# Kernel tuning notes

Hardware: AMD Instinct MI355X
Metric: run time of the kernel (lower is better)

The kernel has to match this reference:

```python
import jax, jax.numpy as jnp
import numpy as np

# Intersection(mode='product'):
#   a_fk = a @ feats.T            # [Na, K]
#   b_fk = b @ feats.T            # [Nb, K]
#   mask = (a_fk[:,None,:] > 0) & (b_fk[None,:,:] > 0)
#   result = sum_k (a_fk[:,None,:] * b_fk[None,:,:]) * mask   # [Na, Nb]
# For the product op, (x*y)*[x>0 & y>0] == relu(x)*relu(y) elementwise
# (any term with a non-positive factor is zeroed either way), so the
# broadcast+mask+reduce collapses exactly into a GEMM over relu'd scores.

def setup_inputs() -> dict:
    key = jax.random.key(0)
    k1, k2, k3 = jax.random.split(key, 3)
    a = jax.random.normal(k1, (1024, 2048), dtype=jnp.float32)
    b = jax.random.normal(k2, (1024, 2048), dtype=jnp.float32)
    feats = jax.random.normal(k3, (128, 2048), dtype=jnp.float32)
    return {"a": a, "b": b, "feats": feats}

def reference(a, b, feats):
    a_fk = a @ feats.T            # [Na, K]
    b_fk = b @ feats.T            # [Nb, K]
    # masked product-intersection reduced over K; identical math to the
    # broadcast (Na, Nb, K) -> sum formulation of the torch module.
    return jnp.einsum('ak,bk->ab', jax.nn.relu(a_fk), jax.nn.relu(b_fk))
```

## Files before the change

### kernel.cpp

```cpp
#include <hip/hip_runtime.h>


typedef __attribute__((ext_vector_type(8))) __bf16 bf16x8;
typedef __attribute__((ext_vector_type(4))) __bf16 bf16x4;
typedef __attribute__((ext_vector_type(4))) float floatx4;

#define KD     2048
#define NF     128
#define NA     1024
#define NPART  16
#define FKN    (2048 * 128)

static __device__ inline bf16x8 cvt8(float4 u, float4 v) {
    bf16x8 s;
    s[0] = (__bf16)u.x; s[1] = (__bf16)u.y; s[2] = (__bf16)u.z; s[3] = (__bf16)u.w;
    s[4] = (__bf16)v.x; s[5] = (__bf16)v.y; s[6] = (__bf16)v.z; s[7] = (__bf16)v.w;
    return s;
}

__global__ __launch_bounds__(256) void gemm1_part(const float* __restrict__ A,
                                                  const float* __restrict__ B,
                                                  const float* __restrict__ F,
                                                  float* __restrict__ part) {
    __shared__ __bf16 Xs[64 * 40];
    __shared__ __bf16 Fs[128 * 40];

    const int t    = threadIdx.x;
    const int m0   = blockIdx.x * 64;
    const int s    = blockIdx.y;
    const int k0   = s * 128;
    const float* src = (m0 < NA) ? (A + (size_t)m0 * KD)
                                 : (B + (size_t)(m0 - NA) * KD);

    const int lane = t & 63;
    const int w    = t >> 6;
    const int ln   = lane & 15;
    const int quad = lane >> 4;
    const int q8   = quad * 8;

    floatx4 acc[4][2];
#pragma unroll
    for (int mt = 0; mt < 4; mt++)
#pragma unroll
        for (int nt = 0; nt < 2; nt++)
            acc[mt][nt] = (floatx4){0.f, 0.f, 0.f, 0.f};

    const int xrow = t >> 2, xcol = (t & 3) * 8;
    const int frow = t >> 1, fcol = (t & 1) * 16;

#pragma unroll
    for (int kk = 0; kk < 128; kk += 32) {
        {
            const float* p = src + (size_t)xrow * KD + (k0 + kk + xcol);
            float4 u = *(const float4*)p;
            float4 v = *(const float4*)(p + 4);
            *(bf16x8*)&Xs[xrow * 40 + xcol] = cvt8(u, v);
        }
        {
            const float* p = F + (size_t)frow * KD + (k0 + kk + fcol);
            float4 u0 = *(const float4*)(p + 0);
            float4 u1 = *(const float4*)(p + 4);
            float4 u2 = *(const float4*)(p + 8);
            float4 u3 = *(const float4*)(p + 12);
            *(bf16x8*)&Fs[frow * 40 + fcol]     = cvt8(u0, u1);
            *(bf16x8*)&Fs[frow * 40 + fcol + 8] = cvt8(u2, u3);
        }
        __syncthreads();

        bf16x8 bfrag[2];
#pragma unroll
        for (int nt = 0; nt < 2; nt++)
            bfrag[nt] = *(const bf16x8*)&Fs[(w * 32 + nt * 16 + ln) * 40 + q8];
#pragma unroll
        for (int mt = 0; mt < 4; mt++) {
            bf16x8 af = *(const bf16x8*)&Xs[(mt * 16 + ln) * 40 + q8];
#pragma unroll
            for (int nt = 0; nt < 2; nt++)
                acc[mt][nt] = __builtin_amdgcn_mfma_f32_16x16x32_bf16(
                    af, bfrag[nt], acc[mt][nt], 0, 0, 0);
        }
        __syncthreads();
    }

    float* pdst = part + (size_t)s * FKN;
#pragma unroll
    for (int mt = 0; mt < 4; mt++)
#pragma unroll
        for (int nt = 0; nt < 2; nt++)
#pragma unroll
            for (int r = 0; r < 4; r++) {
                int row = m0 + mt * 16 + quad * 4 + r;
                int col = w * 32 + nt * 16 + ln;
                pdst[(size_t)row * NF + col] = acc[mt][nt][r];
            }
}

__global__ __launch_bounds__(256) void reduce_relu(const float* __restrict__ part,
                                                   __bf16* __restrict__ fkb) {
    int idx = blockIdx.x * 256 + threadIdx.x;
    size_t base = (size_t)idx * 4;
    float4 sum = make_float4(0.f, 0.f, 0.f, 0.f);
#pragma unroll
    for (int s = 0; s < NPART; s++) {
        float4 u = *(const float4*)(part + (size_t)s * FKN + base);
        sum.x += u.x; sum.y += u.y; sum.z += u.z; sum.w += u.w;
    }
    bf16x4 o;
    o[0] = (__bf16)fmaxf(sum.x, 0.f);
    o[1] = (__bf16)fmaxf(sum.y, 0.f);
    o[2] = (__bf16)fmaxf(sum.z, 0.f);
    o[3] = (__bf16)fmaxf(sum.w, 0.f);
    *(bf16x4*)(fkb + base) = o;
}

__global__ __launch_bounds__(256) void gemm2(const __bf16* __restrict__ fkb,
                                             float* __restrict__ out) {
    __shared__ __bf16 Ps[64 * 136];
    __shared__ __bf16 Qs[64 * 136];

    const int t    = threadIdx.x;
    const int i0   = blockIdx.y * 64;
    const int j0   = blockIdx.x * 64;
    const int lane = t & 63;
    const int w    = t >> 6;
    const int wm   = w & 1;
    const int wn   = w >> 1;
    const int ln   = lane & 15;
    const int quad = lane >> 4;
    const int q8   = quad * 8;

    const int prow = t >> 2, pcol = (t & 3) * 32;
    {
        const __bf16* p = fkb + (size_t)(i0 + prow) * NF + pcol;
        const __bf16* q = fkb + (size_t)(NA + j0 + prow) * NF + pcol;
#pragma unroll
        for (int c = 0; c < 32; c += 8) {
            *(bf16x8*)&Ps[prow * 136 + pcol + c] = *(const bf16x8*)(p + c);
            *(bf16x8*)&Qs[prow * 136 + pcol + c] = *(const bf16x8*)(q + c);
        }
    }
    __syncthreads();

    floatx4 acc[2][2];
#pragma unroll
    for (int mt = 0; mt < 2; mt++)
#pragma unroll
        for (int nt = 0; nt < 2; nt++)
            acc[mt][nt] = (floatx4){0.f, 0.f, 0.f, 0.f};

#pragma unroll
    for (int k0 = 0; k0 < 128; k0 += 32) {
        bf16x8 af[2], bf[2];
#pragma unroll
        for (int mt = 0; mt < 2; mt++)
            af[mt] = *(const bf16x8*)&Ps[(wm * 32 + mt * 16 + ln) * 136 + k0 + q8];
#pragma unroll
        for (int nt = 0; nt < 2; nt++)
            bf[nt] = *(const bf16x8*)&Qs[(wn * 32 + nt * 16 + ln) * 136 + k0 + q8];
#pragma unroll
        for (int mt = 0; mt < 2; mt++)
#pragma unroll
            for (int nt = 0; nt < 2; nt++)
                acc[mt][nt] = __builtin_amdgcn_mfma_f32_16x16x32_bf16(
                    af[mt], bf[nt], acc[mt][nt], 0, 0, 0);
    }

#pragma unroll
    for (int mt = 0; mt < 2; mt++)
#pragma unroll
        for (int nt = 0; nt < 2; nt++)
#pragma unroll
            for (int r = 0; r < 4; r++) {
                int row = i0 + wm * 32 + mt * 16 + quad * 4 + r;
                int col = j0 + wn * 32 + nt * 16 + ln;
                out[(size_t)row * 1024 + col] = acc[mt][nt][r];
            }
}

extern "C" void kernel_launch(void* const* d_in, const int* in_sizes, int n_in,
                              void* d_out, int out_size, void* d_ws, size_t ws_size,
                              hipStream_t stream) {
    const float* a     = (const float*)d_in[0];
    const float* b     = (const float*)d_in[1];
    const float* feats = (const float*)d_in[2];
    float* out = (float*)d_out;

    float*   part = (float*)d_ws;
    __bf16*  fkb  = (__bf16*)((char*)d_ws + (size_t)NPART * FKN * 4);

    gemm1_part<<<dim3(32, NPART), 256, 0, stream>>>(a, b, feats, part);
    reduce_relu<<<256, 256, 0, stream>>>(part, fkb);
    gemm2<<<dim3(16, 16), 256, 0, stream>>>(fkb, out);
}
```

Baseline: 79.36 us.

## Fuse three kernels into one persistent kernel with grid barriers

Merges the split-K projection GEMM, the partial-sum reduction with ReLU, and the output GEMM into a single 256-block, 512-thread kernel. The phases are separated by software grid barriers built on an atomic counter, which is cleared by a memset before launch. The split-K factor drops from 16 to 8, halving the partial-sum traffic. This removes two kernel launches and their gaps, but it relies on all 256 blocks being co-resident and adds spin-wait barrier overhead. It also leaves fewer blocks to parallelise the first GEMM.

New measurement: 121.7 us. +53.4%, slower.

```diff
diff --git a/kernel.cpp b/kernel.cpp
--- a/kernel.cpp
+++ b/kernel.cpp
@@ -3,14 +3,22 @@
 
 typedef __attribute__((ext_vector_type(8))) __bf16 bf16x8;
 typedef __attribute__((ext_vector_type(4))) __bf16 bf16x4;
+typedef __attribute__((ext_vector_type(2))) __bf16 bf16x2;
 typedef __attribute__((ext_vector_type(4))) float floatx4;
 
 #define KD     2048
 #define NF     128
 #define NA     1024
-#define NPART  16
+#define NPART  8
+#define KSPLIT 256
 #define FKN    (2048 * 128)
+#define NBLK   256
 
+static __device__ inline bf16x4 cvt4(float4 u) {
+    bf16x4 s;
+    s[0] = (__bf16)u.x; s[1] = (__bf16)u.y; s[2] = (__bf16)u.z; s[3] = (__bf16)u.w;
+    return s;
+}
 static __device__ inline bf16x8 cvt8(float4 u, float4 v) {
     bf16x8 s;
     s[0] = (__bf16)u.x; s[1] = (__bf16)u.y; s[2] = (__bf16)u.z; s[3] = (__bf16)u.w;
@@ -18,163 +26,143 @@
     return s;
 }
 
-__global__ __launch_bounds__(256) void gemm1_part(const float* __restrict__ A,
-                                                  const float* __restrict__ B,
-                                                  const float* __restrict__ F,
-                                                  float* __restrict__ part) {
-    __shared__ __bf16 Xs[64 * 40];
-    __shared__ __bf16 Fs[128 * 40];
+static __device__ inline void grid_barrier(unsigned* ctr) {
+    __syncthreads();
+    if (threadIdx.x == 0) {
+        __threadfence();
+        atomicAdd(ctr, 1u);
+        while (__hip_atomic_load(ctr, __ATOMIC_RELAXED, __HIP_MEMORY_SCOPE_AGENT) < NBLK)
+            __builtin_amdgcn_s_sleep(2);
+        __threadfence();
+    }
+    __syncthreads();
+}
 
+union SMem {
+    struct { __bf16 Xs[64 * 40];  __bf16 Fs[128 * 40]; } a;
+    struct { __bf16 Ps[64 * 136]; __bf16 Qs[64 * 136]; } c;
+};
+
+__global__ __launch_bounds__(512) void fused(const float* __restrict__ A,
+                                             const float* __restrict__ B,
+                                             const float* __restrict__ F,
+                                             float* __restrict__ part,
+                                             __bf16* __restrict__ fkb,
+                                             float* __restrict__ out,
+                                             unsigned* __restrict__ ctr) {
+    __shared__ SMem sm;
     const int t    = threadIdx.x;
-    const int m0   = blockIdx.x * 64;
-    const int s    = blockIdx.y;
-    const int k0   = s * 128;
-    const float* src = (m0 < NA) ? (A + (size_t)m0 * KD)
-                                 : (B + (size_t)(m0 - NA) * KD);
-
+    const int b    = blockIdx.x;
     const int lane = t & 63;
     const int w    = t >> 6;
     const int ln   = lane & 15;
     const int quad = lane >> 4;
     const int q8   = quad * 8;
 
-    floatx4 acc[4][2];
+    {
+        const int mtile = b & 31;
+        const int split = b >> 5;
+        const int m0    = mtile * 64;
+        const int k0    = split * KSPLIT;
+        const float* src = (m0 < NA) ? (A + (size_t)m0 * KD)
+                                     : (B + (size_t)(m0 - NA) * KD);
+
+        floatx4 acc[4];
 #pragma unroll
-    for (int mt = 0; mt < 4; mt++)
+        for (int mt = 0; mt < 4; mt++) acc[mt] = (floatx4){0.f, 0.f, 0.f, 0.f};
+
+        const int xrow = t >> 3, xcol = (t & 7) * 4;
+        const int frow = t >> 2, fcol = (t & 3) * 8;
+
+        for (int kk = 0; kk < KSPLIT; kk += 32) {
+            {
+                float4 u = *(const float4*)(src + (size_t)xrow * KD + (k0 + kk + xcol));
+                *(bf16x4*)&sm.a.Xs[xrow * 40 + xcol] = cvt4(u);
+            }
+            {
+                const float* p = F + (size_t)frow * KD + (k0 + kk + fcol);
+                float4 u = *(const float4*)p;
+                float4 v = *(const float4*)(p + 4);
+                *(bf16x8*)&sm.a.Fs[frow * 40 + fcol] = cvt8(u, v);
+            }
+            __syncthreads();
+
+            bf16x8 bfrag = *(const bf16x8*)&sm.a.Fs[(w * 16 + ln) * 40 + q8];
 #pragma unroll
-        for (int nt = 0; nt < 2; nt++)
-            acc[mt][nt] = (floatx4){0.f, 0.f, 0.f, 0.f};
+            for (int mt = 0; mt < 4; mt++) {
+                bf16x8 af = *(const bf16x8*)&sm.a.Xs[(mt * 16 + ln) * 40 + q8];
+                acc[mt] = __builtin_amdgcn_mfma_f32_16x16x32_bf16(af, bfrag, acc[mt], 0, 0, 0);
+            }
+            __syncthreads();
+        }
 
-    const int xrow = t >> 2, xcol = (t & 3) * 8;
-    const int frow = t >> 1, fcol = (t & 1) * 16;
+        float* pdst = part + (size_t)split * FKN;
+        const int col = w * 16 + ln;
+#pragma unroll
+        for (int mt = 0; mt < 4; mt++)
+#pragma unroll
+            for (int r = 0; r < 4; r++)
+                pdst[(size_t)(m0 + mt * 16 + quad * 4 + r) * NF + col] = acc[mt][r];
+    }
 
+    grid_barrier(ctr);
+
+    {
+        size_t base = ((size_t)b << 10) + (size_t)t * 2;
+        float sx = 0.f, sy = 0.f;
 #pragma unroll
-    for (int kk = 0; kk < 128; kk += 32) {
+        for (int s = 0; s < NPART; s++) {
+            float2 u = *(const float2*)(part + (size_t)s * FKN + base);
+            sx += u.x; sy += u.y;
+        }
+        bf16x2 o;
+        o[0] = (__bf16)fmaxf(sx, 0.f);
+        o[1] = (__bf16)fmaxf(sy, 0.f);
+        *(bf16x2*)(fkb + base) = o;
+    }
+
+    grid_barrier(ctr + 32);
+
+    {
+        const int i0 = (b >> 4) * 64;
+        const int j0 = (b & 15) * 64;
+        const int wm = w & 1;
+        const int wn = w >> 1;
+
+        const int prow = t >> 3, pcol = (t & 7) * 16;
         {
-            const float* p = src + (size_t)xrow * KD + (k0 + kk + xcol);
-            float4 u = *(const float4*)p;
-            float4 v = *(const float4*)(p + 4);
-            *(bf16x8*)&Xs[xrow * 40 + xcol] = cvt8(u, v);
-        }
-        {
-            const float* p = F + (size_t)frow * KD + (k0 + kk + fcol);
-            float4 u0 = *(const float4*)(p + 0);
-            float4 u1 = *(const float4*)(p + 4);
-            float4 u2 = *(const float4*)(p + 8);
-            float4 u3 = *(const float4*)(p + 12);
-            *(bf16x8*)&Fs[frow * 40 + fcol]     = cvt8(u0, u1);
-            *(bf16x8*)&Fs[frow * 40 + fcol + 8] = cvt8(u2, u3);
+            const __bf16* p = fkb + (size_t)(i0 + prow) * NF + pcol;
+            const __bf16* q = fkb + (size_t)(NA + j0 + prow) * NF + pcol;
+            *(bf16x8*)&sm.c.Ps[prow * 136 + pcol]     = *(const bf16x8*)p;
+            *(bf16x8*)&sm.c.Ps[prow * 136 + pcol + 8] = *(const bf16x8*)(p + 8);
+            *(bf16x8*)&sm.c.Qs[prow * 136 + pcol]     = *(const bf16x8*)q;
+            *(bf16x8*)&sm.c.Qs[prow * 136 + pcol + 8] = *(const bf16x8*)(q + 8);
         }
         __syncthreads();
 
-        bf16x8 bfrag[2];
+        floatx4 acc[2];
 #pragma unroll
-        for (int nt = 0; nt < 2; nt++)
-            bfrag[nt] = *(const bf16x8*)&Fs[(w * 32 + nt * 16 + ln) * 40 + q8];
-#pragma unroll
-        for (int mt = 0; mt < 4; mt++) {
-            bf16x8 af = *(const bf16x8*)&Xs[(mt * 16 + ln) * 40 + q8];
-#pragma unroll
-            for (int nt = 0; nt < 2; nt++)
-                acc[mt][nt] = __builtin_amdgcn_mfma_f32_16x16x32_bf16(
-                    af, bfrag[nt], acc[mt][nt], 0, 0, 0);
-        }
-        __syncthreads();
-    }
-
-    float* pdst = part + (size_t)s * FKN;
-#pragma unroll
-    for (int mt = 0; mt < 4; mt++)
-#pragma unroll
-        for (int nt = 0; nt < 2; nt++)
-#pragma unroll
-            for (int r = 0; r < 4; r++) {
-                int row = m0 + mt * 16 + quad * 4 + r;
-                int col = w * 32 + nt * 16 + ln;
-                pdst[(size_t)row * NF + col] = acc[mt][nt][r];
-            }
-}
-
-__global__ __launch_bounds__(256) void reduce_relu(const float* __restrict__ part,
-                                                   __bf16* __restrict__ fkb) {
-    int idx = blockIdx.x * 256 + threadIdx.x;
-    size_t base = (size_t)idx * 4;
-    float4 sum = make_float4(0.f, 0.f, 0.f, 0.f);
-#pragma unroll
-    for (int s = 0; s < NPART; s++) {
-        float4 u = *(const float4*)(part + (size_t)s * FKN + base);
-        sum.x += u.x; sum.y += u.y; sum.z += u.z; sum.w += u.w;
-    }
-    bf16x4 o;
-    o[0] = (__bf16)fmaxf(sum.x, 0.f);
-    o[1] = (__bf16)fmaxf(sum.y, 0.f);
-    o[2] = (__bf16)fmaxf(sum.z, 0.f);
-    o[3] = (__bf16)fmaxf(sum.w, 0.f);
-    *(bf16x4*)(fkb + base) = o;
-}
-
-__global__ __launch_bounds__(256) void gemm2(const __bf16* __restrict__ fkb,
-                                             float* __restrict__ out) {
-    __shared__ __bf16 Ps[64 * 136];
-    __shared__ __bf16 Qs[64 * 136];
-
-    const int t    = threadIdx.x;
-    const int i0   = blockIdx.y * 64;
-    const int j0   = blockIdx.x * 64;
-    const int lane = t & 63;
-    const int w    = t >> 6;
-    const int wm   = w & 1;
-    const int wn   = w >> 1;
-    const int ln   = lane & 15;
-    const int quad = lane >> 4;
-    const int q8   = quad * 8;
-
-    const int prow = t >> 2, pcol = (t & 3) * 32;
-    {
-        const __bf16* p = fkb + (size_t)(i0 + prow) * NF + pcol;
-        const __bf16* q = fkb + (size_t)(NA + j0 + prow) * NF + pcol;
-#pragma unroll
-        for (int c = 0; c < 32; c += 8) {
-            *(bf16x8*)&Ps[prow * 136 + pcol + c] = *(const bf16x8*)(p + c);
-            *(bf16x8*)&Qs[prow * 136 + pcol + c] = *(const bf16x8*)(q + c);
-        }
-    }
-    __syncthreads();
-
-    floatx4 acc[2][2];
-#pragma unroll
-    for (int mt = 0; mt < 2; mt++)
-#pragma unroll
-        for (int nt = 0; nt < 2; nt++)
-            acc[mt][nt] = (floatx4){0.f, 0.f, 0.f, 0.f};
+        for (int mt = 0; mt < 2; mt++) acc[mt] = (floatx4){0.f, 0.f, 0.f, 0.f};
 
 #pragma unroll
-    for (int k0 = 0; k0 < 128; k0 += 32) {
-        bf16x8 af[2], bf[2];
+        for (int k0 = 0; k0 < NF; k0 += 32) {
+            bf16x8 bf = *(const bf16x8*)&sm.c.Qs[(wn * 16 + ln) * 136 + k0 + q8];
 #pragma unroll
-        for (int mt = 0; mt < 2; mt++)
-            af[mt] = *(const bf16x8*)&Ps[(wm * 32 + mt * 16 + ln) * 136 + k0 + q8];
-#pragma unroll
-        for (int nt = 0; nt < 2; nt++)
-            bf[nt] = *(const bf16x8*)&Qs[(wn * 32 + nt * 16 + ln) * 136 + k0 + q8];
+            for (int mt = 0; mt < 2; mt++) {
+                bf16x8 af = *(const bf16x8*)&sm.c.Ps[(wm * 32 + mt * 16 + ln) * 136 + k0 + q8];
+                acc[mt] = __builtin_amdgcn_mfma_f32_16x16x32_bf16(af, bf, acc[mt], 0, 0, 0);
+            }
+        }
+
 #pragma unroll
         for (int mt = 0; mt < 2; mt++)
 #pragma unroll
-            for (int nt = 0; nt < 2; nt++)
-                acc[mt][nt] = __builtin_amdgcn_mfma_f32_16x16x32_bf16(
-                    af[mt], bf[nt], acc[mt][nt], 0, 0, 0);
-    }
-
-#pragma unroll
-    for (int mt = 0; mt < 2; mt++)
-#pragma unroll
-        for (int nt = 0; nt < 2; nt++)
-#pragma unroll
             for (int r = 0; r < 4; r++) {
                 int row = i0 + wm * 32 + mt * 16 + quad * 4 + r;
-                int col = j0 + wn * 32 + nt * 16 + ln;
-                out[(size_t)row * 1024 + col] = acc[mt][nt][r];
+                int col = j0 + wn * 16 + ln;
+                out[(size_t)row * 1024 + col] = acc[mt][r];
             }
+    }
 }
 
 extern "C" void kernel_launch(void* const* d_in, const int* in_sizes, int n_in,
@@ -185,10 +173,10 @@
     const float* feats = (const float*)d_in[2];
     float* out = (float*)d_out;
 
-    float*   part = (float*)d_ws;
-    __bf16*  fkb  = (__bf16*)((char*)d_ws + (size_t)NPART * FKN * 4);
+    float*    part = (float*)d_ws;
+    __bf16*   fkb  = (__bf16*)((char*)d_ws + (size_t)NPART * FKN * 4);
+    unsigned* ctr  = (unsigned*)((char*)d_ws + (size_t)NPART * FKN * 4 + (size_t)FKN * 2);
 
-    gemm1_part<<<dim3(32, NPART), 256, 0, stream>>>(a, b, feats, part);
-    reduce_relu<<<256, 256, 0, stream>>>(part, fkb);
-    gemm2<<<dim3(16, 16), 256, 0, stream>>>(fkb, out);
+    hipMemsetAsync(ctr, 0, 256, stream);
+    fused<<<NBLK, 512, 0, stream>>>(a, b, feats, part, fkb, out, ctr);
 }
```

## Fuse split-K reduction into gemm1 via last-block atomic counter

Applied to the files above, without the earlier changes.

Removes the separate reduce_relu kernel. The last split-K block to finish each 64-row tile, found with an atomic counter, sums the partials and writes relu'd bf16 scores. The gemm1 inner tile is also widened from BK=32 to BK=64, which halves the number of barrier pairs per block. In exchange it adds a memset launch for the counters, threadfences, and a serialized reduction tail on the last block of each tile.

Measured after the change: 104.9 us. +32.2%, slower.

```diff
diff --git a/kernel.cpp b/kernel.cpp
--- a/kernel.cpp
+++ b/kernel.cpp
@@ -8,8 +8,11 @@
 #define KD     2048
 #define NF     128
 #define NA     1024
-#define NPART  16
+#define NSPLIT 16
+#define KSP    128
+#define BK     64
 #define FKN    (2048 * 128)
+#define XSTR   72
 
 static __device__ inline bf16x8 cvt8(float4 u, float4 v) {
     bf16x8 s;
@@ -17,27 +20,34 @@
     s[4] = (__bf16)v.x; s[5] = (__bf16)v.y; s[6] = (__bf16)v.z; s[7] = (__bf16)v.w;
     return s;
 }
-
-__global__ __launch_bounds__(256) void gemm1_part(const float* __restrict__ A,
-                                                  const float* __restrict__ B,
-                                                  const float* __restrict__ F,
-                                                  float* __restrict__ part) {
-    __shared__ __bf16 Xs[64 * 40];
-    __shared__ __bf16 Fs[128 * 40];
+static __device__ inline void acc4(float4& d, float4 u) {
+    d.x += u.x; d.y += u.y; d.z += u.z; d.w += u.w;
+}
+
+__global__ __launch_bounds__(256) void gemm1(const float* __restrict__ A,
+                                             const float* __restrict__ B,
+                                             const float* __restrict__ F,
+                                             float* __restrict__ part,
+                                             unsigned* __restrict__ ctr,
+                                             __bf16* __restrict__ fkb) {
+    __shared__ __bf16 Xs[64 * XSTR];
+    __shared__ __bf16 Fs[128 * XSTR];
+    __shared__ int isred;
 
     const int t    = threadIdx.x;
-    const int m0   = blockIdx.x * 64;
-    const int s    = blockIdx.y;
-    const int k0   = s * 128;
-    const float* src = (m0 < NA) ? (A + (size_t)m0 * KD)
-                                 : (B + (size_t)(m0 - NA) * KD);
-
     const int lane = t & 63;
     const int w    = t >> 6;
     const int ln   = lane & 15;
     const int quad = lane >> 4;
     const int q8   = quad * 8;
 
+    const int mtile = blockIdx.x;
+    const int m0    = mtile * 64;
+    const int s     = blockIdx.y;
+    const int k0    = s * KSP;
+    const float* src = (m0 < NA) ? (A + (size_t)m0 * KD)
+                                 : (B + (size_t)(m0 - NA) * KD);
+
     floatx4 acc[4][2];
 #pragma unroll
     for (int mt = 0; mt < 4; mt++)
@@ -45,39 +55,48 @@
         for (int nt = 0; nt < 2; nt++)
             acc[mt][nt] = (floatx4){0.f, 0.f, 0.f, 0.f};
 
-    const int xrow = t >> 2, xcol = (t & 3) * 8;
-    const int frow = t >> 1, fcol = (t & 1) * 16;
-
-#pragma unroll
-    for (int kk = 0; kk < 128; kk += 32) {
+    const int xr = t >> 2, xc = (t & 3) * 16;
+    const int fr = t >> 1, fc = (t & 1) * 32;
+
+#pragma unroll
+    for (int kk = 0; kk < KSP; kk += BK) {
         {
-            const float* p = src + (size_t)xrow * KD + (k0 + kk + xcol);
-            float4 u = *(const float4*)p;
-            float4 v = *(const float4*)(p + 4);
-            *(bf16x8*)&Xs[xrow * 40 + xcol] = cvt8(u, v);
-        }
-        {
-            const float* p = F + (size_t)frow * KD + (k0 + kk + fcol);
+            const float* p = src + (size_t)xr * KD + (k0 + kk + xc);
             float4 u0 = *(const float4*)(p + 0);
             float4 u1 = *(const float4*)(p + 4);
             float4 u2 = *(const float4*)(p + 8);
             float4 u3 = *(const float4*)(p + 12);
-            *(bf16x8*)&Fs[frow * 40 + fcol]     = cvt8(u0, u1);
-            *(bf16x8*)&Fs[frow * 40 + fcol + 8] = cvt8(u2, u3);
+            *(bf16x8*)&Xs[xr * XSTR + xc]     = cvt8(u0, u1);
+            *(bf16x8*)&Xs[xr * XSTR + xc + 8] = cvt8(u2, u3);
+        }
+        {
+            const float* p = F + (size_t)fr * KD + (k0 + kk + fc);
+#pragma unroll
+            for (int j = 0; j < 32; j += 16) {
+                float4 u0 = *(const float4*)(p + j + 0);
+                float4 u1 = *(const float4*)(p + j + 4);
+                float4 u2 = *(const float4*)(p + j + 8);
+                float4 u3 = *(const float4*)(p + j + 12);
+                *(bf16x8*)&Fs[fr * XSTR + fc + j]     = cvt8(u0, u1);
+                *(bf16x8*)&Fs[fr * XSTR + fc + j + 8] = cvt8(u2, u3);
+            }
         }
         __syncthreads();
 
-        bf16x8 bfrag[2];
-#pragma unroll
-        for (int nt = 0; nt < 2; nt++)
-            bfrag[nt] = *(const bf16x8*)&Fs[(w * 32 + nt * 16 + ln) * 40 + q8];
-#pragma unroll
-        for (int mt = 0; mt < 4; mt++) {
-            bf16x8 af = *(const bf16x8*)&Xs[(mt * 16 + ln) * 40 + q8];
+#pragma unroll
+        for (int ks = 0; ks < BK; ks += 32) {
+            bf16x8 bfrag[2];
 #pragma unroll
             for (int nt = 0; nt < 2; nt++)
-                acc[mt][nt] = __builtin_amdgcn_mfma_f32_16x16x32_bf16(
-                    af, bfrag[nt], acc[mt][nt], 0, 0, 0);
+                bfrag[nt] = *(const bf16x8*)&Fs[(w * 32 + nt * 16 + ln) * XSTR + ks + q8];
+#pragma unroll
+            for (int mt = 0; mt < 4; mt++) {
+                bf16x8 af = *(const bf16x8*)&Xs[(mt * 16 + ln) * XSTR + ks + q8];
+#pragma unroll
+                for (int nt = 0; nt < 2; nt++)
+                    acc[mt][nt] = __builtin_amdgcn_mfma_f32_16x16x32_bf16(
+                        af, bfrag[nt], acc[mt][nt], 0, 0, 0);
+            }
         }
         __syncthreads();
     }
@@ -88,29 +107,39 @@
 #pragma unroll
         for (int nt = 0; nt < 2; nt++)
 #pragma unroll
-            for (int r = 0; r < 4; r++) {
-                int row = m0 + mt * 16 + quad * 4 + r;
-                int col = w * 32 + nt * 16 + ln;
-                pdst[(size_t)row * NF + col] = acc[mt][nt][r];
-            }
-}
-
-__global__ __launch_bounds__(256) void reduce_relu(const float* __restrict__ part,
-                                                   __bf16* __restrict__ fkb) {
-    int idx = blockIdx.x * 256 + threadIdx.x;
-    size_t base = (size_t)idx * 4;
-    float4 sum = make_float4(0.f, 0.f, 0.f, 0.f);
-#pragma unroll
-    for (int s = 0; s < NPART; s++) {
-        float4 u = *(const float4*)(part + (size_t)s * FKN + base);
-        sum.x += u.x; sum.y += u.y; sum.z += u.z; sum.w += u.w;
-    }
-    bf16x4 o;
-    o[0] = (__bf16)fmaxf(sum.x, 0.f);
-    o[1] = (__bf16)fmaxf(sum.y, 0.f);
-    o[2] = (__bf16)fmaxf(sum.z, 0.f);
-    o[3] = (__bf16)fmaxf(sum.w, 0.f);
-    *(bf16x4*)(fkb + base) = o;
+            for (int r = 0; r < 4; r++)
+                pdst[(size_t)(m0 + mt * 16 + quad * 4 + r) * NF
+                     + (w * 32 + nt * 16 + ln)] = acc[mt][nt][r];
+
+    __syncthreads();
+    if (t == 0) {
+        __threadfence();
+        unsigned old = __hip_atomic_fetch_add(&ctr[mtile * 32], 1u,
+                           __ATOMIC_RELAXED, __HIP_MEMORY_SCOPE_AGENT);
+        int red = (old == NSPLIT - 1);
+        if (red) __threadfence();
+        isred = red;
+    }
+    __syncthreads();
+    if (!isred) return;
+
+#pragma unroll
+    for (int i = 0; i < 8; i++) {
+        int f   = i * 256 + t;
+        int row = f >> 5;
+        int c4  = (f & 31) * 4;
+        size_t off = (size_t)(m0 + row) * NF + c4;
+        float4 sum = make_float4(0.f, 0.f, 0.f, 0.f);
+#pragma unroll
+        for (int ss = 0; ss < NSPLIT; ss++)
+            acc4(sum, *(const float4*)(part + (size_t)ss * FKN + off));
+        bf16x4 o;
+        o[0] = (__bf16)fmaxf(sum.x, 0.f);
+        o[1] = (__bf16)fmaxf(sum.y, 0.f);
+        o[2] = (__bf16)fmaxf(sum.z, 0.f);
+        o[3] = (__bf16)fmaxf(sum.w, 0.f);
+        *(bf16x4*)(fkb + off) = o;
+    }
 }
 
 __global__ __launch_bounds__(256) void gemm2(const __bf16* __restrict__ fkb,
@@ -149,7 +178,7 @@
             acc[mt][nt] = (floatx4){0.f, 0.f, 0.f, 0.f};
 
 #pragma unroll
-    for (int k0 = 0; k0 < 128; k0 += 32) {
+    for (int k0 = 0; k0 < NF; k0 += 32) {
         bf16x8 af[2], bf[2];
 #pragma unroll
         for (int mt = 0; mt < 2; mt++)
@@ -185,10 +214,11 @@
     const float* feats = (const float*)d_in[2];
     float* out = (float*)d_out;
 
-    float*   part = (float*)d_ws;
-    __bf16*  fkb  = (__bf16*)((char*)d_ws + (size_t)NPART * FKN * 4);
-
-    gemm1_part<<<dim3(32, NPART), 256, 0, stream>>>(a, b, feats, part);
-    reduce_relu<<<256, 256, 0, stream>>>(part, fkb);
+    float*    part = (float*)d_ws;
+    unsigned* ctr  = (unsigned*)((char*)d_ws + (size_t)NSPLIT * FKN * 4);
+    __bf16*   fkb  = (__bf16*)((char*)d_ws + (size_t)NSPLIT * FKN * 4 + 8192);
+
+    hipMemsetAsync(ctr, 0, 4096, stream);
+    gemm1<<<dim3(32, NSPLIT), 256, 0, stream>>>(a, b, feats, part, ctr, fkb);
     gemm2<<<dim3(16, 16), 256, 0, stream>>>(fkb, out);
 }
```
